# Performance work log

Hardware: AMD Instinct MI355X
Metric: run time of the kernel (lower is better)

Reference implementation:

```python
import jax, jax.numpy as jnp
import numpy as np

B, N, D, H, DFF = 2, 2048, 1024, 16, 4096
HD = D // H
L = 3
WINDOWS = (256, 64, 16)   # sliding-window size per hierarchy level
LEVEL_SCALE = 16          # pos_l = token_idx // LEVEL_SCALE**l
EPS = 1e-5
NEG = -1e9


def setup_inputs() -> dict:
    key = jax.random.key(0)
    ks = jax.random.split(key, 16)
    s = 0.02
    x = jax.random.normal(ks[0], (B, N, D), dtype=jnp.float32)
    idx = jnp.arange(N, dtype=jnp.int32)
    positions = jnp.stack([idx // (LEVEL_SCALE ** l) for l in range(L)], axis=0)  # [L, N]
    return {
        "x": x,
        "positions": positions,
        "w_qkv": jax.random.normal(ks[1], (D, 3 * D), dtype=jnp.float32) * s,
        "b_qkv": jnp.zeros((3 * D,), dtype=jnp.float32),
        "w_out": jax.random.normal(ks[2], (D, D), dtype=jnp.float32) * s,
        "b_out": jnp.zeros((D,), dtype=jnp.float32),
        "w_ff1": jax.random.normal(ks[3], (D, DFF), dtype=jnp.float32) * s,
        "b_ff1": jnp.zeros((DFF,), dtype=jnp.float32),
        "w_ff2": jax.random.normal(ks[4], (DFF, D), dtype=jnp.float32) * s,
        "b_ff2": jnp.zeros((D,), dtype=jnp.float32),
        "g1": jnp.ones((D,), dtype=jnp.float32),
        "beta1": jnp.zeros((D,), dtype=jnp.float32),
        "g2": jnp.ones((D,), dtype=jnp.float32),
        "beta2": jnp.zeros((D,), dtype=jnp.float32),
    }


def _layernorm(x, g, b):
    m = jnp.mean(x, axis=-1, keepdims=True)
    v = jnp.var(x, axis=-1, keepdims=True)
    return (x - m) * jax.lax.rsqrt(v + EPS) * g + b


def _mlswa_mask(positions):
    # union over levels of per-level sliding windows: |pos_l[i]-pos_l[j]| < w_l
    allowed = jnp.zeros((N, N), dtype=bool)
    for l, w in enumerate(WINDOWS):
        p = positions[l]
        allowed = allowed | (jnp.abs(p[:, None] - p[None, :]) < w)
    return allowed  # [N, N]


def reference(x, positions, w_qkv, b_qkv, w_out, b_out,
              w_ff1, b_ff1, w_ff2, b_ff2, g1, beta1, g2, beta2):
    residual = x
    xn = _layernorm(x, g1, beta1)
    qkv = xn @ w_qkv + b_qkv                       # [B, N, 3D]
    qkv = qkv.reshape(B, N, 3, H, HD)
    q, k, v = qkv[:, :, 0], qkv[:, :, 1], qkv[:, :, 2]  # [B, N, H, HD]

    scale = 1.0 / np.sqrt(HD)
    scores = jnp.einsum('bihd,bjhd->bhij', q, k) * scale  # [B, H, N, N]
    allowed = _mlswa_mask(positions)
    scores = jnp.where(allowed[None, None], scores, NEG)
    attn = jax.nn.softmax(scores, axis=-1)
    out = jnp.einsum('bhij,bjhd->bihd', attn, v).reshape(B, N, D)
    out = out @ w_out + b_out
    x = residual + out

    residual = x
    xn = _layernorm(x, g2, beta2)
    ff = jax.nn.gelu(xn @ w_ff1 + b_ff1, approximate=False) @ w_ff2 + b_ff2
    return residual + ff
```

## Files before the change

kernel.cpp:

```cpp
#include <hip/hip_runtime.h>
#include <cstdint>
#include <cstddef>


using u16 = unsigned short;
using u32 = unsigned int;

typedef __attribute__((ext_vector_type(8)))  short bf16x8;
typedef __attribute__((ext_vector_type(4)))  float f32x4;
typedef __attribute__((ext_vector_type(16))) float f32x16;

#define DEV __device__ __forceinline__

DEV u16 f2bf(float f) {
  u32 u = __builtin_bit_cast(u32, f);
  u32 r = (u + 0x7FFFu + ((u >> 16) & 1u)) >> 16;
  return (u16)r;
}
DEV float bf2f(u16 u) { return __builtin_bit_cast(float, (u32)u << 16); }
DEV u32 pk2(float a, float b) { return (u32)f2bf(a) | ((u32)f2bf(b) << 16); }
DEV u32 cvtpk(float lo, float hi) {
  u32 r;
  asm("v_cvt_pk_bf16_f32 %0, %1, %2" : "=v"(r) : "v"(lo), "v"(hi));
  return r;
}
DEV float fexp2(float x) { return __builtin_amdgcn_exp2f(x); }

DEV void gload_lds16(const void* g, void* lds) {
  __builtin_amdgcn_global_load_lds(
      (const __attribute__((address_space(1))) u32*)g,
      (__attribute__((address_space(3))) u32*)lds, 16, 0, 0);
}

DEV float fast_gelu(float x) {
  float u = x * fmaf(0.035677408137f, x * x, 0.7978845608f);
  u = fminf(fmaxf(u, -15.0f), 15.0f);
  float e = fexp2(u * 2.885390081777927f);
  return x * e * __builtin_amdgcn_rcpf(e + 1.0f);
}

__global__ __launch_bounds__(256) void k_transpose_bf16(const float* __restrict__ in,
                                                        u16* __restrict__ out, int R, int C) {
  __shared__ float ts[32][33];
  int n0 = blockIdx.x * 32, r0 = blockIdx.y * 32;
  int t = threadIdx.x;
  int c = t & 31, r = t >> 5;
#pragma unroll
  for (int j = 0; j < 4; ++j)
    ts[r + 8 * j][c] = in[(size_t)(r0 + r + 8 * j) * C + n0 + c];
  __syncthreads();
#pragma unroll
  for (int j = 0; j < 4; ++j)
    out[(size_t)(n0 + r + 8 * j) * R + r0 + c] = f2bf(ts[c][r + 8 * j]);
}

__global__ __launch_bounds__(256) void k_layernorm(const float* __restrict__ x,
                                                   const float* __restrict__ g,
                                                   const float* __restrict__ be,
                                                   u16* __restrict__ o) {
  int row = blockIdx.x;
  int t = threadIdx.x;
  const float* xr = x + (size_t)row * 1024;
  f32x4 v = *(const f32x4*)(xr + t * 4);
  float s = v[0] + v[1] + v[2] + v[3];
  float s2 = v[0] * v[0] + v[1] * v[1] + v[2] * v[2] + v[3] * v[3];
#pragma unroll
  for (int off = 1; off < 64; off <<= 1) {
    s += __shfl_xor(s, off);
    s2 += __shfl_xor(s2, off);
  }
  __shared__ float red[8];
  if ((t & 63) == 0) { red[t >> 6] = s; red[4 + (t >> 6)] = s2; }
  __syncthreads();
  s = red[0] + red[1] + red[2] + red[3];
  s2 = red[4] + red[5] + red[6] + red[7];
  float mean = s * (1.0f / 1024.0f);
  float var = fmaxf(s2 * (1.0f / 1024.0f) - mean * mean, 0.0f);
  float rstd = rsqrtf(var + 1e-5f);
  f32x4 gg = *(const f32x4*)(g + t * 4);
  f32x4 bb = *(const f32x4*)(be + t * 4);
  uint2 ww;
  ww.x = pk2((v[0] - mean) * rstd * gg[0] + bb[0], (v[1] - mean) * rstd * gg[1] + bb[1]);
  ww.y = pk2((v[2] - mean) * rstd * gg[2] + bb[2], (v[3] - mean) * rstd * gg[3] + bb[3]);
  *(uint2*)(o + (size_t)row * 1024 + t * 4) = ww;
}

template <int MODE, int SPLIT>
__global__ __launch_bounds__(SPLIT * 256) void k_gemm(
    const u16* __restrict__ A, const u16* __restrict__ Bt, int K, int NC,
    const float* __restrict__ bias, const float* __restrict__ resid,
    void* __restrict__ o0, void* __restrict__ o1, void* __restrict__ o2) {
  __shared__ u16 tiles[SPLIT][2][128 * 64];
  const int lane = threadIdx.x & 63, wave = threadIdx.x >> 6;
  const int group = (SPLIT == 2) ? (wave >> 2) : 0;
  const int wv = wave & 3;
  const int nwg = gridDim.x * gridDim.y;
  const int id = blockIdx.y * gridDim.x + blockIdx.x;
  const int wg = (id & 7) * (nwg >> 3) + (id >> 3);
  const int tN = (wg % gridDim.x) * 128, tM = (wg / gridDim.x) * 128;
  const int wm = (wv >> 1) * 64, wn = (wv & 1) * 64;
  const int lm = lane & 15, lh = lane >> 4;
  const int K2 = K / SPLIT;
  const int kbase = group * K2;
  f32x4 acc[4][4] = {};

  auto STAGE = [&](int k0) {
#pragma unroll
    for (int i = 0; i < 4; ++i) {
      int seg = i * 4 + wv;
      int li = seg * 64 + lane;
      int m = li >> 3, ch = li & 7;
      gload_lds16(A + (size_t)(tM + m) * K + kbase + k0 + ((ch ^ (m & 7)) << 3),
                  (void*)(tiles[group][0] + seg * 512));
      gload_lds16(Bt + (size_t)(tN + m) * K + kbase + k0 + ((ch ^ (m & 7)) << 3),
                  (void*)(tiles[group][1] + seg * 512));
    }
  };

  const int nk = K2 >> 6;
  for (int t = 0; t < nk; ++t) {
    __syncthreads();
    STAGE(t << 6);
    __syncthreads();
#pragma unroll
    for (int s = 0; s < 2; ++s) {
      bf16x8 af[4], bfr[4];
#pragma unroll
      for (int i = 0; i < 4; ++i) {
        int m = wm + i * 16 + lm;
        af[i] = *(const bf16x8*)((const char*)tiles[group][0] + m * 128 +
                                 (((s * 4 + lh) ^ (m & 7)) << 4));
      }
#pragma unroll
      for (int j = 0; j < 4; ++j) {
        int n = wn + j * 16 + lm;
        bfr[j] = *(const bf16x8*)((const char*)tiles[group][1] + n * 128 +
                                  (((s * 4 + lh) ^ (n & 7)) << 4));
      }
#pragma unroll
      for (int i = 0; i < 4; ++i)
#pragma unroll
        for (int j = 0; j < 4; ++j)
          acc[i][j] = __builtin_amdgcn_mfma_f32_16x16x32_bf16(af[i], bfr[j], acc[i][j], 0, 0, 0);
    }
  }

  if constexpr (SPLIT == 2) {
    float* comb = (float*)tiles;
    __syncthreads();
    if (group == 1) {
#pragma unroll
      for (int i = 0; i < 4; ++i)
#pragma unroll
        for (int j = 0; j < 4; ++j)
          *(f32x4*)&comb[(i * 4 + j) * 1024 + wv * 256 + lane * 4] = acc[i][j];
    }
    __syncthreads();
    if (group == 1) return;
#pragma unroll
    for (int i = 0; i < 4; ++i)
#pragma unroll
      for (int j = 0; j < 4; ++j) {
        f32x4 other = *(const f32x4*)&comb[(i * 4 + j) * 1024 + wv * 256 + lane * 4];
#pragma unroll
        for (int r = 0; r < 4; ++r) acc[i][j][r] += other[r];
      }
  }

#pragma unroll
  for (int i = 0; i < 4; ++i) {
#pragma unroll
    for (int j = 0; j < 4; ++j) {
      int gn = tN + wn + j * 16 + lm;
      int gm0 = tM + wm + i * 16 + lh * 4;
      float vals[4];
#pragma unroll
      for (int r = 0; r < 4; ++r) vals[r] = acc[i][j][r] + bias[gn];
      if constexpr (MODE == 0) {
        int which = gn >> 10, h = (gn >> 6) & 15, d = gn & 63;
        int b = gm0 >> 11, nn0 = gm0 & 2047;
        if (which == 2) {
          uint2 w2;
          w2.x = pk2(vals[0], vals[1]);
          w2.y = pk2(vals[2], vals[3]);
          *(uint2*)((u16*)o2 + ((size_t)(b * 16 + h) * 64 + d) * 2048 + nn0) = w2;
        } else {
          u16* dst = which == 0 ? (u16*)o0 : (u16*)o1;
          float sc = which == 0 ? 0.125f : 1.0f;
#pragma unroll
          for (int r = 0; r < 4; ++r)
            dst[(((size_t)(b * 16 + h)) * 2048 + nn0 + r) * 64 + d] = f2bf(vals[r] * sc);
        }
      } else if constexpr (MODE == 2) {
#pragma unroll
        for (int r = 0; r < 4; ++r)
          ((u16*)o0)[(size_t)(gm0 + r) * NC + gn] = f2bf(fast_gelu(vals[r]));
      } else {
#pragma unroll
        for (int r = 0; r < 4; ++r)
          ((float*)o0)[(size_t)(gm0 + r) * NC + gn] =
              vals[r] + resid[(size_t)(gm0 + r) * NC + gn];
      }
    }
  }
}

__global__ __launch_bounds__(256) void k_attn(const u16* __restrict__ q,
                                              const u16* __restrict__ k,
                                              const u16* __restrict__ vt,
                                              u16* __restrict__ o) {
  __shared__ u16 KT[2][4096];
  __shared__ u16 VT[2][4096];
  const int tid = threadIdx.x;
  const int lane = tid & 63, wave = tid >> 6;
  const int ql = lane & 31, hi = lane >> 5;
  const int id = blockIdx.y * 16 + blockIdx.x;
  const int wg = (id & 7) * 64 + (id >> 3);
  const int qb = wg & 15, bh = wg >> 4;
  const int q0 = qb * 128 + wave * 32;
  const float C_LOG2E = 1.44269504088896f;
  const float MSHIFT = 8.0f * C_LOG2E;

  const u16* qp = q + ((size_t)bh * 2048 + q0 + ql) * 64 + hi * 8;
  bf16x8 qf[4];
#pragma unroll
  for (int dc = 0; dc < 4; ++dc) qf[dc] = *(const bf16x8*)(qp + dc * 16);

  const u16* kst = k + (size_t)bh * 2048 * 64;
  const u16* vst = vt + (size_t)bh * 64 * 2048;

  f32x16 ot0 = {0, 0, 0, 0, 0, 0, 0, 0, 0, 0, 0, 0, 0, 0, 0, 0};
  f32x16 ot1 = ot0;
  float lsum = 0.0f;

  u32 koffA[4], koffB[4], voffA[4], voffB[4];
#pragma unroll
  for (int dc = 0; dc < 4; ++dc) {
    u32 sw = (((u32)((dc << 1) | hi) ^ (ql & 7)) << 3);
    koffA[dc] = (ql << 6) + sw;
    koffB[dc] = ((32 + ql) << 6) + sw;
  }
#pragma unroll
  for (int kc = 0; kc < 2; ++kc)
#pragma unroll
    for (int dh = 0; dh < 2; ++dh) {
      u32 rb = ((u32)((dh << 5) + ql) << 6);
      voffA[kc * 2 + dh] = rb + ((((kc << 1) + hi) ^ (ql & 7)) << 3);
      voffB[kc * 2 + dh] = rb + (((4 + (kc << 1) + hi) ^ (ql & 7)) << 3);
    }

  auto STAGE = [&](int tl, int b) {
    int kb = tl << 6;
#pragma unroll
    for (int i = 0; i < 2; ++i) {
      int seg = i * 4 + wave;
      int li = seg * 64 + lane;
      int row = li >> 3, ch = li & 7;
      int sw = (ch ^ (row & 7)) << 3;
      gload_lds16(kst + (size_t)(kb + row) * 64 + sw, (void*)&KT[b][seg * 512]);
      gload_lds16(vst + (size_t)row * 2048 + kb + sw, (void*)&VT[b][seg * 512]);
    }
  };

  auto COMPUTE = [&](const u16* KTb, const u16* VTb) {
    f32x16 st0 = {0, 0, 0, 0, 0, 0, 0, 0, 0, 0, 0, 0, 0, 0, 0, 0};
    f32x16 st1 = st0;
    bf16x8 kfa[4], kfb[4];
#pragma unroll
    for (int dc = 0; dc < 4; ++dc) {
      kfa[dc] = *(const bf16x8*)(KTb + koffA[dc]);
      kfb[dc] = *(const bf16x8*)(KTb + koffB[dc]);
    }
    __builtin_amdgcn_s_setprio(1);
#pragma unroll
    for (int dc = 0; dc < 4; ++dc) {
      st0 = __builtin_amdgcn_mfma_f32_32x32x16_bf16(kfa[dc], qf[dc], st0, 0, 0, 0);
      st1 = __builtin_amdgcn_mfma_f32_32x32x16_bf16(kfb[dc], qf[dc], st1, 0, 0, 0);
    }
    __builtin_amdgcn_s_setprio(0);
    bf16x8 vf0[4], vf1[4];
#pragma unroll
    for (int i = 0; i < 4; ++i) {
      vf0[i] = *(const bf16x8*)(VTb + voffA[i]);
      vf1[i] = *(const bf16x8*)(VTb + voffB[i]);
    }
    float p0[16], p1v[16];
#pragma unroll
    for (int r = 0; r < 16; ++r) {
      p0[r] = fexp2(fmaf(st0[r], C_LOG2E, -MSHIFT));
      p1v[r] = fexp2(fmaf(st1[r], C_LOG2E, -MSHIFT));
    }
    float s8[8];
#pragma unroll
    for (int r = 0; r < 8; ++r)
      s8[r] = (p0[2 * r] + p0[2 * r + 1]) + (p1v[2 * r] + p1v[2 * r + 1]);
#pragma unroll
    for (int r = 0; r < 4; ++r) s8[r] = s8[r] + s8[r + 4];
    float ts = (s8[0] + s8[2]) + (s8[1] + s8[3]);
    {
      float p1 = ts, p2 = ts;
      asm("v_permlane32_swap_b32 %0, %1" : "+v"(p1), "+v"(p2));
      ts = p1 + p2;
    }
    lsum += ts;
    __builtin_amdgcn_s_setprio(1);
#pragma unroll
    for (int kc = 0; kc < 2; ++kc) {
      u32 x0 = cvtpk(p0[kc * 8 + 0], p0[kc * 8 + 1]), x1 = cvtpk(p0[kc * 8 + 2], p0[kc * 8 + 3]);
      u32 y0 = cvtpk(p0[kc * 8 + 4], p0[kc * 8 + 5]), y1 = cvtpk(p0[kc * 8 + 6], p0[kc * 8 + 7]);
      asm("v_permlane32_swap_b32 %0, %1" : "+v"(x0), "+v"(y0));
      asm("v_permlane32_swap_b32 %0, %1" : "+v"(x1), "+v"(y1));
      union { u32 u[4]; bf16x8 v8; } pf;
      pf.u[0] = x0; pf.u[1] = x1; pf.u[2] = y0; pf.u[3] = y1;
      ot0 = __builtin_amdgcn_mfma_f32_32x32x16_bf16(vf0[kc * 2 + 0], pf.v8, ot0, 0, 0, 0);
      ot1 = __builtin_amdgcn_mfma_f32_32x32x16_bf16(vf0[kc * 2 + 1], pf.v8, ot1, 0, 0, 0);
    }
#pragma unroll
    for (int kc = 0; kc < 2; ++kc) {
      u32 x0 = cvtpk(p1v[kc * 8 + 0], p1v[kc * 8 + 1]), x1 = cvtpk(p1v[kc * 8 + 2], p1v[kc * 8 + 3]);
      u32 y0 = cvtpk(p1v[kc * 8 + 4], p1v[kc * 8 + 5]), y1 = cvtpk(p1v[kc * 8 + 6], p1v[kc * 8 + 7]);
      asm("v_permlane32_swap_b32 %0, %1" : "+v"(x0), "+v"(y0));
      asm("v_permlane32_swap_b32 %0, %1" : "+v"(x1), "+v"(y1));
      union { u32 u[4]; bf16x8 v8; } pf;
      pf.u[0] = x0; pf.u[1] = x1; pf.u[2] = y0; pf.u[3] = y1;
      ot0 = __builtin_amdgcn_mfma_f32_32x32x16_bf16(vf1[kc * 2 + 0], pf.v8, ot0, 0, 0, 0);
      ot1 = __builtin_amdgcn_mfma_f32_32x32x16_bf16(vf1[kc * 2 + 1], pf.v8, ot1, 0, 0, 0);
    }
    __builtin_amdgcn_s_setprio(0);
  };

  STAGE(0, 0);
  __syncthreads();

#pragma unroll 1
  for (int t2 = 0; t2 < 16; ++t2) {
    const int tlA = t2 * 2;
    STAGE(tlA + 1, 1);
    COMPUTE(KT[0], VT[0]);
    __syncthreads();
    if (t2 < 15) STAGE(tlA + 2, 0);
    COMPUTE(KT[1], VT[1]);
    __syncthreads();
  }

  float inv = 1.0f / lsum;
  int b = bh >> 4, h = bh & 15;
  size_t ob = ((size_t)b * 2048 + q0 + ql) * 1024 + h * 64;
#pragma unroll
  for (int r = 0; r < 16; ++r) {
    int d = (r & 3) + ((r >> 2) << 3) + hi * 4;
    o[ob + d] = f2bf(ot0[r] * inv);
    o[ob + 32 + d] = f2bf(ot1[r] * inv);
  }
}

extern "C" void kernel_launch(void* const* d_in, const int* in_sizes, int n_in,
                              void* d_out, int out_size, void* d_ws, size_t ws_size,
                              hipStream_t stream) {
  const float* x = (const float*)d_in[0];
  const float* w_qkv = (const float*)d_in[2];
  const float* b_qkv = (const float*)d_in[3];
  const float* w_out = (const float*)d_in[4];
  const float* b_out = (const float*)d_in[5];
  const float* w_ff1 = (const float*)d_in[6];
  const float* b_ff1 = (const float*)d_in[7];
  const float* w_ff2 = (const float*)d_in[8];
  const float* b_ff2 = (const float*)d_in[9];
  const float* g1 = (const float*)d_in[10];
  const float* be1 = (const float*)d_in[11];
  const float* g2 = (const float*)d_in[12];
  const float* be2 = (const float*)d_in[13];
  float* out = (float*)d_out;

  char* wp = (char*)d_ws;
  u16* wqkvT = (u16*)wp; wp += (size_t)3072 * 1024 * 2;
  u16* woutT = (u16*)wp; wp += (size_t)1024 * 1024 * 2;
  u16* wff1T = (u16*)wp; wp += (size_t)4096 * 1024 * 2;
  u16* wff2T = (u16*)wp; wp += (size_t)1024 * 4096 * 2;
  u16* xn    = (u16*)wp; wp += (size_t)4096 * 1024 * 2;
  float* x2  = (float*)wp; wp += (size_t)4096 * 1024 * 4;
  u16* qbuf  = (u16*)wp; wp += (size_t)32 * 2048 * 64 * 2;
  u16* kbuf  = (u16*)wp; wp += (size_t)32 * 2048 * 64 * 2;
  u16* vtbuf = (u16*)wp; wp += (size_t)32 * 2048 * 64 * 2;
  u16* attnb = (u16*)wp; wp += (size_t)4096 * 1024 * 2;
  u16* ffh   = qbuf;

  k_transpose_bf16<<<dim3(3072 / 32, 1024 / 32), 256, 0, stream>>>(w_qkv, wqkvT, 1024, 3072);
  k_transpose_bf16<<<dim3(1024 / 32, 1024 / 32), 256, 0, stream>>>(w_out, woutT, 1024, 1024);
  k_transpose_bf16<<<dim3(4096 / 32, 1024 / 32), 256, 0, stream>>>(w_ff1, wff1T, 1024, 4096);
  k_transpose_bf16<<<dim3(1024 / 32, 4096 / 32), 256, 0, stream>>>(w_ff2, wff2T, 4096, 1024);

  k_layernorm<<<4096, 256, 0, stream>>>(x, g1, be1, xn);
  k_gemm<0, 2><<<dim3(24, 32), 512, 0, stream>>>(xn, wqkvT, 1024, 3072, b_qkv, nullptr,
                                                 qbuf, kbuf, vtbuf);
  k_attn<<<dim3(16, 32), 256, 0, stream>>>(qbuf, kbuf, vtbuf, attnb);
  k_gemm<1, 2><<<dim3(8, 32), 512, 0, stream>>>(attnb, woutT, 1024, 1024, b_out, x,
                                                x2, nullptr, nullptr);
  k_layernorm<<<4096, 256, 0, stream>>>(x2, g2, be2, xn);
  k_gemm<2, 2><<<dim3(32, 32), 512, 0, stream>>>(xn, wff1T, 1024, 4096, b_ff1, nullptr,
                                                 ffh, nullptr, nullptr);
  k_gemm<3, 2><<<dim3(8, 32), 512, 0, stream>>>(ffh, wff2T, 4096, 1024, b_ff2, x2,
                                                out, nullptr, nullptr);
}
```

Baseline: 250.0 us.

## Use four-way intra-block split-K for the FF2 GEMM with tree reduction

The FF2 GEMM (K=4096, only 256 blocks) now runs with four wave groups per block, each taking a quarter of K, in 1024-thread blocks. Partial accumulators are combined through LDS in a pairwise tree reduction, and each group writes one row-slice of the epilogue with bias and residual added. The aim is more latency hiding and more waves per block for this under-occupied GEMM. In exchange it costs extra LDS traffic and barriers, and the larger blocks with 64KB LDS may limit residency.

```diff
diff --git a/kernel.cpp b/kernel.cpp
--- a/kernel.cpp
+++ b/kernel.cpp
@@ -92,7 +92,7 @@
     void* __restrict__ o0, void* __restrict__ o1, void* __restrict__ o2) {
   __shared__ u16 tiles[SPLIT][2][128 * 64];
   const int lane = threadIdx.x & 63, wave = threadIdx.x >> 6;
-  const int group = (SPLIT == 2) ? (wave >> 2) : 0;
+  const int group = (SPLIT >= 2) ? (wave >> 2) : 0;
   const int wv = wave & 3;
   const int nwg = gridDim.x * gridDim.y;
   const int id = blockIdx.y * gridDim.x + blockIdx.x;
@@ -145,26 +145,62 @@
     }
   }
 
+  auto dumpacc = [&](float* c) {
+#pragma unroll
+    for (int i = 0; i < 4; ++i)
+#pragma unroll
+      for (int j = 0; j < 4; ++j)
+        *(f32x4*)&c[(i * 4 + j) * 1024 + wv * 256 + lane * 4] = acc[i][j];
+  };
+  auto addacc = [&](const float* c) {
+#pragma unroll
+    for (int i = 0; i < 4; ++i)
+#pragma unroll
+      for (int j = 0; j < 4; ++j) {
+        f32x4 o4 = *(const f32x4*)&c[(i * 4 + j) * 1024 + wv * 256 + lane * 4];
+#pragma unroll
+        for (int r = 0; r < 4; ++r) acc[i][j][r] += o4[r];
+      }
+  };
+
+  if constexpr (SPLIT == 4) {
+    float* cA = (float*)&tiles[0][0][0];
+    float* cB = (float*)&tiles[2][0][0];
+    __syncthreads();
+    if (group == 1) dumpacc(cA);
+    if (group == 3) dumpacc(cB);
+    __syncthreads();
+    if (group == 0) addacc(cA);
+    if (group == 2) addacc(cB);
+    __syncthreads();
+    if (group == 2) dumpacc(cA);
+    __syncthreads();
+    if (group == 0) { addacc(cA); dumpacc(cB); }
+    __syncthreads();
+    {
+      const int i = group;
+#pragma unroll
+      for (int j = 0; j < 4; ++j) {
+        int gn = tN + wn + j * 16 + lm;
+        int gm0 = tM + wm + i * 16 + lh * 4;
+        f32x4 v4 = *(const f32x4*)&cB[(i * 4 + j) * 1024 + wv * 256 + lane * 4];
+        float bv = bias[gn];
+#pragma unroll
+        for (int r = 0; r < 4; ++r)
+          ((float*)o0)[(size_t)(gm0 + r) * NC + gn] =
+              v4[r] + bv + resid[(size_t)(gm0 + r) * NC + gn];
+      }
+    }
+    return;
+  }
+
   if constexpr (SPLIT == 2) {
     float* comb = (float*)tiles;
     __syncthreads();
-    if (group == 1) {
-#pragma unroll
-      for (int i = 0; i < 4; ++i)
-#pragma unroll
-        for (int j = 0; j < 4; ++j)
-          *(f32x4*)&comb[(i * 4 + j) * 1024 + wv * 256 + lane * 4] = acc[i][j];
-    }
+    if (group == 1) dumpacc(comb);
     __syncthreads();
     if (group == 1) return;
-#pragma unroll
-    for (int i = 0; i < 4; ++i)
-#pragma unroll
-      for (int j = 0; j < 4; ++j) {
-        f32x4 other = *(const f32x4*)&comb[(i * 4 + j) * 1024 + wv * 256 + lane * 4];
-#pragma unroll
-        for (int r = 0; r < 4; ++r) acc[i][j][r] += other[r];
-      }
+    addacc(comb);
   }
 
 #pragma unroll
@@ -399,6 +435,6 @@
   k_layernorm<<<4096, 256, 0, stream>>>(x2, g2, be2, xn);
   k_gemm<2, 2><<<dim3(32, 32), 512, 0, stream>>>(xn, wff1T, 1024, 4096, b_ff1, nullptr,
                                                  ffh, nullptr, nullptr);
-  k_gemm<3, 2><<<dim3(8, 32), 512, 0, stream>>>(ffh, wff2T, 4096, 1024, b_ff2, x2,
-                                                out, nullptr, nullptr);
-}
+  k_gemm<3, 4><<<dim3(8, 32), 1024, 0, stream>>>(ffh, wff2T, 4096, 1024, b_ff2, x2,
+                                                 out, nullptr, nullptr);
+}
```

Result: no change. 245.4 us (-1.8%).
